# Kernel tuning notes

Hardware: AMD Instinct MI355X
Metric: run time of the kernel (lower is better)

The kernel has to match this reference:

```python
import jax, jax.numpy as jnp
import numpy as np


def _conv_same(x, w, b):
    # 3x3 same-padding conv, NCHW / OIHW (matches ConvNdWithSamePadding with
    # kernel=3, stride=1, dilation=1 -> symmetric pad of 1)
    y = jax.lax.conv_general_dilated(
        x, w, window_strides=(1, 1), padding='SAME',
        dimension_numbers=('NCHW', 'OIHW', 'NCHW'))
    return y + b[None, :, None, None]


def setup_inputs() -> dict:
    key = jax.random.key(0)
    ks = jax.random.split(key, 5)
    B, A, C, H, W = 8, 6, 256, 32, 32
    x = jax.random.normal(ks[0], (B, A, C, H, W), dtype=jnp.float32)
    w_ih = jax.random.normal(ks[1], (3 * C, 2 * C, 3, 3), dtype=jnp.float32) * 0.02
    w_hh = jax.random.normal(ks[2], (3 * C, C, 3, 3), dtype=jnp.float32) * 0.02
    b_ih = jax.random.normal(ks[3], (3 * C,), dtype=jnp.float32) * 0.02
    b_hh = jax.random.normal(ks[4], (3 * C,), dtype=jnp.float32) * 0.02
    return {'x': x, 'w_ih': w_ih, 'w_hh': w_hh, 'b_ih': b_ih, 'b_hh': b_hh,
            'num_iters': 3}


def reference(x, w_ih, w_hh, b_ih, b_hh, num_iters):
    # x: [B, A, C, H, W] per-agent BEV features.
    # Each GNN iteration: message = mean of other agents' features,
    # GRU input = concat(own, message) [2C ch], hidden = own feature [C ch],
    # new feature = ConvGRU cell output.
    B, A, C, H, W = x.shape
    for _ in range(num_iters):
        # mean over the other A-1 agents, computed via total sum (vectorized)
        msg = (jnp.sum(x, axis=1, keepdims=True) - x) / (A - 1)
        inp = jnp.concatenate([x, msg], axis=2).reshape(B * A, 2 * C, H, W)
        h = x.reshape(B * A, C, H, W)
        gi = _conv_same(inp, w_ih, b_ih)   # [B*A, 3C, H, W]
        gh = _conv_same(h, w_hh, b_hh)     # [B*A, 3C, H, W]
        i_r, i_i, i_n = jnp.split(gi, 3, axis=1)
        h_r, h_i, h_n = jnp.split(gh, 3, axis=1)
        resetgate = jax.nn.sigmoid(i_r + h_r)
        inputgate = jax.nn.sigmoid(i_i + h_i)
        newgate = jnp.tanh(i_n + resetgate * h_n)
        hy = newgate + inputgate * (h - newgate)
        x = hy.reshape(B, A, C, H, W)
    return x
```

## Files before the change

### kernel.cpp

```cpp
#include <hip/hip_runtime.h>
#include <stdint.h>

typedef unsigned short u16;
typedef __attribute__((ext_vector_type(8))) short short8;
typedef __attribute__((ext_vector_type(4))) float f32x4;

__device__ __forceinline__ u16 f2bf(float f) {
  uint32_t u = __builtin_bit_cast(uint32_t, f);
  u += 0x7fffu + ((u >> 16) & 1u);
  return (u16)(u >> 16);
}

__device__ __forceinline__ void gld16(const void* g, void* l) {
  __builtin_amdgcn_global_load_lds(
      (const __attribute__((address_space(1))) void*)g,
      (__attribute__((address_space(3))) void*)l, 16, 0, 0);
}

__device__ __forceinline__ void waitv(int n) {
  switch (n) {
    case 0: asm volatile("s_waitcnt vmcnt(0)" ::: "memory"); break;
    case 1: asm volatile("s_waitcnt vmcnt(1)" ::: "memory"); break;
    case 2: asm volatile("s_waitcnt vmcnt(2)" ::: "memory"); break;
    case 3: asm volatile("s_waitcnt vmcnt(3)" ::: "memory"); break;
    case 4: asm volatile("s_waitcnt vmcnt(4)" ::: "memory"); break;
    case 5: asm volatile("s_waitcnt vmcnt(5)" ::: "memory"); break;
    default: asm volatile("s_waitcnt vmcnt(6)" ::: "memory"); break;
  }
}

__global__ __launch_bounds__(256) void k_wprep(const float* __restrict__ w_ih,
                                               const float* __restrict__ w_hh,
                                               u16* __restrict__ wA,
                                               u16* __restrict__ wS) {
  const int NA = 8*9*8*192*32;
  const int NS = 8*9*8*96*32;
  for (int idx = blockIdx.x*blockDim.x + threadIdx.x; idx < NA + NS;
       idx += gridDim.x*blockDim.x) {
    if (idx < NA) {
      int kk = idx & 31; int t = idx >> 5;
      int nl = t % 192; t /= 192;
      int kb = t & 7; t >>= 3;
      int tap = t % 9; int cb = t / 9;
      int qq = nl / 96; int rr = nl % 96;
      int g = rr >> 4, cl = rr & 15;
      int c = cb*32 + qq*16 + cl, ci = kb*32 + kk;
      float v;
      if (g < 3) {
        int o = g*256 + c;
        v = w_ih[(o*512 + ci)*9 + tap] - 0.2f * w_ih[(o*512 + 256 + ci)*9 + tap];
      } else {
        int o = (g-3)*256 + c;
        v = w_hh[(o*256 + ci)*9 + tap];
      }
      wA[idx] = f2bf(v);
    } else {
      int j = idx - NA;
      int kk = j & 31; int t = j >> 5;
      int nl = t % 96; t /= 96;
      int kb = t & 7; t >>= 3;
      int tap = t % 9; int cb = t / 9;
      int o = cb*96 + nl, ci = kb*32 + kk;
      wS[j] = f2bf(0.2f * w_ih[(o*512 + 256 + ci)*9 + tap]);
    }
  }
}

__global__ __launch_bounds__(256) void k_xform(const float* __restrict__ src,
                                               u16* __restrict__ xbf,
                                               u16* __restrict__ sbf) {
  __shared__ float lds[32][33];
  const int t = threadIdx.x;
  const int tx = t & 31, ty = t >> 5;
  const int p0 = blockIdx.x*32, c0 = blockIdx.y*32, b = blockIdx.z;
  const int po = t >> 3, co = (t & 7)*4;
  float ss[4] = {0.f,0.f,0.f,0.f};
  for (int a = 0; a < 6; ++a) {
    const int im = b*6 + a;
    const float* sp = src + ((size_t)im*256 + c0)*1024 + p0;
    #pragma unroll
    for (int k = 0; k < 4; ++k) {
      float v = sp[(size_t)(ty + 8*k)*1024 + tx];
      ss[k] += v;
      lds[ty + 8*k][tx] = v;
    }
    __syncthreads();
    ushort4 pk = make_ushort4(f2bf(lds[co+0][po]), f2bf(lds[co+1][po]),
                              f2bf(lds[co+2][po]), f2bf(lds[co+3][po]));
    *(ushort4*)(xbf + ((size_t)im*1024 + p0+po)*256 + c0 + co) = pk;
    __syncthreads();
  }
  #pragma unroll
  for (int k = 0; k < 4; ++k) lds[ty + 8*k][tx] = ss[k];
  __syncthreads();
  ushort4 pk = make_ushort4(f2bf(lds[co+0][po]), f2bf(lds[co+1][po]),
                            f2bf(lds[co+2][po]), f2bf(lds[co+3][po]));
  *(ushort4*)(sbf + ((size_t)b*1024 + p0+po)*256 + c0 + co) = pk;
}

template<int GF, bool GATES>
__global__ __launch_bounds__(512, 2)
void k_conv(const u16* __restrict__ xin, const u16* __restrict__ wpre,
            float* __restrict__ gsbuf,
            const float* __restrict__ b_ih, const float* __restrict__ b_hh,
            const float* __restrict__ h_in, float* __restrict__ h_out) {
  constexpr int NT   = 512;
  constexpr int SLAB = 10*32*32;
  constexpr int BN   = 2*GF*16*32;
  constexpr int TOTA = 10*128;
  constexpr int TOTB = BN/8;
  __shared__ __align__(16) u16 slab[2][SLAB];
  __shared__ __align__(16) u16 bbuf[3][BN];

  const int tid = threadIdx.x;
  const int l  = tid & 63;
  const int w  = tid >> 6;
  const int lx = l & 15;
  const int lk = l >> 4;
  const int rg = w >> 1;
  const int q  = w & 1;

  int bid = blockIdx.x;
  const int cb = bid & 7; bid >>= 3;
  const int mt = bid & 3;
  const int img = bid >> 2;
  const int h0 = mt * 8;

  const u16* srcimg = xin + (size_t)img * (1024*256);

  const int trf = __builtin_amdgcn_readfirstlane(tid);
  const int myB = TOTB/NT + ((trf < (TOTB % NT)) ? 1 : 0);
  const int myA = TOTA/NT + ((trf < (TOTA % NT)) ? 1 : 0);

  auto stageA = [&](int kb, int sbuf) {
    #pragma unroll
    for (int ii = 0; ii < (TOTA + NT - 1)/NT; ++ii) {
      int i = ii*NT + tid;
      if (i < TOTA) {
        int p = i >> 2, ck = i & 3;
        int pr = p >> 5, pc = p & 31;
        int gr = h0 - 1 + pr;
        gr = gr < 0 ? 0 : (gr > 31 ? 31 : gr);
        int sck = ck ^ ((p >> 1) & 3);
        gld16(srcimg + (gr*32 + pc)*256 + kb*32 + sck*8, &slab[sbuf][i*8]);
      }
    }
  };
  auto stageB = [&](int kb, int tap, int bb) {
    const u16* wb = wpre + (size_t)((cb*9 + tap)*8 + kb) * BN;
    #pragma unroll
    for (int ii = 0; ii < (TOTB + NT - 1)/NT; ++ii) {
      int i = ii*NT + tid;
      if (i < TOTB) {
        int nl = i >> 2, ck = i & 3;
        int sck = ck ^ ((nl >> 1) & 3);
        gld16(wb + nl*32 + sck*8, &bbuf[bb][i*8]);
      }
    }
  };

  f32x4 acc[4][GF];
  #pragma unroll
  for (int mi = 0; mi < 4; ++mi)
    #pragma unroll
    for (int g = 0; g < GF; ++g) acc[mi][g] = (f32x4){0.f,0.f,0.f,0.f};

  stageA(0, 0);
  stageB(0, 0, 0);
  stageB(0, 1, 1);

  for (int kb = 0; kb < 8; ++kb) {
    const int sb = kb & 1;
    #pragma unroll
    for (int tap = 0; tap < 9; ++tap) {
      const int tau = kb*9 + tap;
      if (tau == 71) waitv(0);
      else if (tap == 7 && kb < 7) waitv(myA + myB);
      else waitv(myB);
      __builtin_amdgcn_s_barrier();
      __builtin_amdgcn_sched_barrier(0);

      if (tap == 6 && kb < 7) stageA(kb+1, sb^1);
      if (tau <= 69) stageB((tau+2)/9, (tau+2)%9, (tau+2)%3);

      const int dy = tap/3, dx = tap%3;
      short8 a[4];
      #pragma unroll
      for (int mi = 0; mi < 4; ++mi) {
        const int grow = h0 + rg*2 + (mi>>1) + dy - 1;
        const int cc = (mi&1)*16 + lx + dx - 1;
        const bool ok = (grow >= 0) && (grow < 32) && (cc >= 0) && (cc < 32);
        const int ccc = cc < 0 ? 0 : (cc > 31 ? 31 : cc);
        const int sr = rg*2 + (mi>>1) + dy;
        short8 av = *(const short8*)&slab[sb][(sr*32 + ccc)*32 + (lk ^ ((ccc >> 1) & 3))*8];
        if (!ok) av = (short8){0,0,0,0,0,0,0,0};
        a[mi] = av;
      }
      const u16* bp = &bbuf[tau % 3][(q*(GF*16) + lx)*32 + (lk ^ ((lx >> 1) & 3))*8];
      __builtin_amdgcn_s_setprio(1);
      #pragma unroll
      for (int g = 0; g < GF; ++g) {
        short8 bv = *(const short8*)(bp + g*(16*32));
        #pragma unroll
        for (int mi = 0; mi < 4; ++mi)
          acc[mi][g] = __builtin_amdgcn_mfma_f32_16x16x32_bf16(a[mi], bv, acc[mi][g], 0, 0, 0);
      }
      __builtin_amdgcn_s_setprio(0);
    }
  }

  if constexpr (GATES) {
    const int b = img / 6;
    const int c = cb*32 + q*16 + lx;
    const float bir = b_ih[c],  bii = b_ih[256+c], bin_ = b_ih[512+c];
    const float bhr = b_hh[c],  bhi = b_hh[256+c], bhn  = b_hh[512+c];
    const float* gs0 = gsbuf + ((size_t)(b*3+0)*256 + c)*1024;
    const float* gs1 = gsbuf + ((size_t)(b*3+1)*256 + c)*1024;
    const float* gs2 = gsbuf + ((size_t)(b*3+2)*256 + c)*1024;
    const float* hp  = h_in  + ((size_t)img*256 + c)*1024;
    float*       op  = h_out + ((size_t)img*256 + c)*1024;
    #pragma unroll
    for (int mi = 0; mi < 4; ++mi) {
      const int R = h0 + rg*2 + (mi>>1);
      const int pix = R*32 + (mi&1)*16 + lk*4;
      float4 v0 = *(const float4*)(gs0 + pix);
      float4 v1 = *(const float4*)(gs1 + pix);
      float4 v2 = *(const float4*)(gs2 + pix);
      float4 hv = *(const float4*)(hp + pix);
      float4 o;
      #pragma unroll
      for (int r = 0; r < 4; ++r) {
        float ir  = acc[mi][0][r] + (&v0.x)[r] + bir;
        float ii  = acc[mi][1][r] + (&v1.x)[r] + bii;
        float inn = acc[mi][2][r] + (&v2.x)[r] + bin_;
        float hr  = acc[mi][3][r] + bhr;
        float hi2 = acc[mi][4][r] + bhi;
        float hn  = acc[mi][5][r] + bhn;
        float rgt = 1.f/(1.f + __expf(-(ir+hr)));
        float igt = 1.f/(1.f + __expf(-(ii+hi2)));
        float nx = inn + rgt*hn;
        nx = nx > 20.f ? 20.f : (nx < -20.f ? -20.f : nx);
        float e2 = __expf(-2.f*nx);
        float ng = (1.f - e2)/(1.f + e2);
        (&o.x)[r] = ng + igt*((&hv.x)[r] - ng);
      }
      *(float4*)(op + pix) = o;
    }
  } else {
    #pragma unroll
    for (int g = 0; g < GF; ++g) {
      const int n = cb*(2*GF*16) + q*(GF*16) + g*16 + lx;
      float* gp = gsbuf + ((size_t)img*768 + n)*1024;
      #pragma unroll
      for (int mi = 0; mi < 4; ++mi) {
        const int R = h0 + rg*2 + (mi>>1);
        const int pix = R*32 + (mi&1)*16 + lk*4;
        *(float4*)(gp + pix) = make_float4(acc[mi][g][0], acc[mi][g][1],
                                           acc[mi][g][2], acc[mi][g][3]);
      }
    }
  }
}

extern "C" void kernel_launch(void* const* d_in, const int* in_sizes, int n_in,
                              void* d_out, int out_size, void* d_ws, size_t ws_size,
                              hipStream_t stream) {
  const float* x    = (const float*)d_in[0];
  const float* w_ih = (const float*)d_in[1];
  const float* w_hh = (const float*)d_in[2];
  const float* b_ih = (const float*)d_in[3];
  const float* b_hh = (const float*)d_in[4];
  float* out = (float*)d_out;

  char* ws = (char*)d_ws;
  float* m0  = (float*)(ws);
  u16*  xbf  = (u16*)(ws + 50331648);
  u16*  sbf  = (u16*)(ws + 75497472);
  float* gsb = (float*)(ws + 79691776);
  u16*  wA   = (u16*)(ws + 104857600);
  u16*  wS   = (u16*)(ws + 111935488);

  k_wprep<<<2048, 256, 0, stream>>>(w_ih, w_hh, wA, wS);

  for (int it = 0; it < 3; ++it) {
    const float* src = (it == 0) ? x : (it == 1 ? out : m0);
    float* dst = (it == 1) ? m0 : out;
    k_xform<<<dim3(32, 8, 8), 256, 0, stream>>>(src, xbf, sbf);
    k_conv<3, false><<<256, 512, 0, stream>>>(sbf, wS, gsb,
                                              nullptr, nullptr, nullptr, nullptr);
    k_conv<6, true><<<1536, 512, 0, stream>>>(xbf, wA, gsb,
                                              b_ih, b_hh, src, dst);
  }
}
```

Before: 1.541 ms.

## Switch conv kernels to 32x32x16 MFMA with larger row tiles and lane-swizzled gates

Replaces the 16x16x32 bf16 MFMA implicit-GEMM conv with a 32x32x16 variant. Each wave now covers a full 32-pixel row and 96 output columns, and the weight layout is reordered so input-gate and hidden-gate columns interleave per 16-channel group. The gated kernel tiles 16 rows per block (768 blocks instead of 1536), halving redundant halo and weight staging. It uses ds_swizzle to exchange ih and hh partial sums between lane halves for the GRU epilogue, and out-of-bounds pixels read from a zeroed LDS pad. The costs are more register pressure from 16-wide accumulators and fewer blocks for latency hiding.

```diff
diff --git a/kernel.cpp b/kernel.cpp
--- a/kernel.cpp
+++ b/kernel.cpp
@@ -3,7 +3,7 @@
 
 typedef unsigned short u16;
 typedef __attribute__((ext_vector_type(8))) short short8;
-typedef __attribute__((ext_vector_type(4))) float f32x4;
+typedef __attribute__((ext_vector_type(16))) float f32x16;
 
 __device__ __forceinline__ u16 f2bf(float f) {
   uint32_t u = __builtin_bit_cast(uint32_t, f);
@@ -25,7 +25,8 @@
     case 3: asm volatile("s_waitcnt vmcnt(3)" ::: "memory"); break;
     case 4: asm volatile("s_waitcnt vmcnt(4)" ::: "memory"); break;
     case 5: asm volatile("s_waitcnt vmcnt(5)" ::: "memory"); break;
-    default: asm volatile("s_waitcnt vmcnt(6)" ::: "memory"); break;
+    case 6: asm volatile("s_waitcnt vmcnt(6)" ::: "memory"); break;
+    default: asm volatile("s_waitcnt vmcnt(7)" ::: "memory"); break;
   }
 }
 
@@ -42,17 +43,15 @@
       int nl = t % 192; t /= 192;
       int kb = t & 7; t >>= 3;
       int tap = t % 9; int cb = t / 9;
-      int qq = nl / 96; int rr = nl % 96;
-      int g = rr >> 4, cl = rr & 15;
-      int c = cb*32 + qq*16 + cl, ci = kb*32 + kk;
+      int nh = nl / 96; int r2 = nl % 96;
+      int p = r2 >> 5, gp = (r2 >> 4) & 1, cl = r2 & 15;
+      int c = cb*32 + nh*16 + cl, ci = kb*32 + kk;
+      int o = p*256 + c;
       float v;
-      if (g < 3) {
-        int o = g*256 + c;
+      if (gp == 0)
         v = w_ih[(o*512 + ci)*9 + tap] - 0.2f * w_ih[(o*512 + 256 + ci)*9 + tap];
-      } else {
-        int o = (g-3)*256 + c;
+      else
         v = w_hh[(o*256 + ci)*9 + tap];
-      }
       wA[idx] = f2bf(v);
     } else {
       int j = idx - NA;
@@ -60,7 +59,8 @@
       int nl = t % 96; t /= 96;
       int kb = t & 7; t >>= 3;
       int tap = t % 9; int cb = t / 9;
-      int o = cb*96 + nl, ci = kb*32 + kk;
+      int p = nl >> 5, cl = nl & 31;
+      int o = p*256 + cb*32 + cl, ci = kb*32 + kk;
       wS[j] = f2bf(0.2f * w_ih[(o*512 + 256 + ci)*9 + tap]);
     }
   }
@@ -98,165 +98,213 @@
   *(ushort4*)(sbf + ((size_t)b*1024 + p0+po)*256 + c0 + co) = pk;
 }
 
-template<int GF, bool GATES>
+template<int MT, int NH, bool GATES>
 __global__ __launch_bounds__(512, 2)
-void k_conv(const u16* __restrict__ xin, const u16* __restrict__ wpre,
-            float* __restrict__ gsbuf,
-            const float* __restrict__ b_ih, const float* __restrict__ b_hh,
-            const float* __restrict__ h_in, float* __restrict__ h_out) {
-  constexpr int NT   = 512;
-  constexpr int SLAB = 10*32*32;
-  constexpr int BN   = 2*GF*16*32;
-  constexpr int TOTA = 10*128;
-  constexpr int TOTB = BN/8;
-  __shared__ __align__(16) u16 slab[2][SLAB];
-  __shared__ __align__(16) u16 bbuf[3][BN];
+void k_conv32(const u16* __restrict__ xin, const u16* __restrict__ wpre,
+              float* __restrict__ gsbuf,
+              const float* __restrict__ b_ih, const float* __restrict__ b_hh,
+              const float* __restrict__ h_in, float* __restrict__ h_out) {
+  constexpr int RGC   = 8 / NH;
+  constexpr int ROWS  = MT * RGC;
+  constexpr int MTC   = 32 / ROWS;
+  constexpr int NBLK  = 96 * NH;
+  constexpr int SLABR = ROWS + 2;
+  constexpr int SLABSZ = SLABR * 1024;
+  constexpr int BBSZ   = NBLK * 32;
+  constexpr int ZOFF   = 2*SLABSZ + 3*BBSZ;
+  constexpr int TOTA   = SLABR * 128;
+  constexpr int TOTB   = NBLK * 4;
+  __shared__ __align__(16) u16 L[ZOFF + 64];
 
   const int tid = threadIdx.x;
-  const int l  = tid & 63;
-  const int w  = tid >> 6;
-  const int lx = l & 15;
-  const int lk = l >> 4;
-  const int rg = w >> 1;
-  const int q  = w & 1;
+  const int l   = tid & 63;
+  const int w   = tid >> 6;
+  const int rg  = w / NH;
+  const int nh  = w % NH;
+  const int colc = l & 31;
+  const int kch  = l >> 5;
 
   int bid = blockIdx.x;
-  const int cb = bid & 7; bid >>= 3;
-  const int mt = bid & 3;
-  const int img = bid >> 2;
-  const int h0 = mt * 8;
+  const int cb  = bid & 7;
+  const int rest = bid >> 3;
+  const int mt  = rest % MTC;
+  const int img = rest / MTC;
+  const int h0  = mt * ROWS;
 
   const u16* srcimg = xin + (size_t)img * (1024*256);
 
   const int trf = __builtin_amdgcn_readfirstlane(tid);
-  const int myB = TOTB/NT + ((trf < (TOTB % NT)) ? 1 : 0);
-  const int myA = TOTA/NT + ((trf < (TOTA % NT)) ? 1 : 0);
+  const int myA = TOTA/512 + ((trf < (TOTA % 512)) ? 1 : 0);
+  const int myB = TOTB/512 + ((trf < (TOTB % 512)) ? 1 : 0);
 
   auto stageA = [&](int kb, int sbuf) {
     #pragma unroll
-    for (int ii = 0; ii < (TOTA + NT - 1)/NT; ++ii) {
-      int i = ii*NT + tid;
+    for (int ii = 0; ii < (TOTA + 511)/512; ++ii) {
+      int i = ii*512 + tid;
       if (i < TOTA) {
         int p = i >> 2, ck = i & 3;
         int pr = p >> 5, pc = p & 31;
         int gr = h0 - 1 + pr;
         gr = gr < 0 ? 0 : (gr > 31 ? 31 : gr);
-        int sck = ck ^ ((p >> 1) & 3);
-        gld16(srcimg + (gr*32 + pc)*256 + kb*32 + sck*8, &slab[sbuf][i*8]);
+        int sck = ck ^ ((pc >> 1) & 3);
+        gld16(srcimg + (gr*32 + pc)*256 + kb*32 + sck*8, &L[sbuf*SLABSZ + i*8]);
       }
     }
   };
   auto stageB = [&](int kb, int tap, int bb) {
-    const u16* wb = wpre + (size_t)((cb*9 + tap)*8 + kb) * BN;
-    #pragma unroll
-    for (int ii = 0; ii < (TOTB + NT - 1)/NT; ++ii) {
-      int i = ii*NT + tid;
+    const u16* wb = wpre + (size_t)((cb*9 + tap)*8 + kb) * BBSZ;
+    #pragma unroll
+    for (int ii = 0; ii < (TOTB + 511)/512; ++ii) {
+      int i = ii*512 + tid;
       if (i < TOTB) {
         int nl = i >> 2, ck = i & 3;
         int sck = ck ^ ((nl >> 1) & 3);
-        gld16(wb + nl*32 + sck*8, &bbuf[bb][i*8]);
+        gld16(wb + nl*32 + sck*8, &L[2*SLABSZ + bb*BBSZ + i*8]);
       }
     }
   };
 
-  f32x4 acc[4][GF];
+  f32x16 acc[MT][3];
   #pragma unroll
-  for (int mi = 0; mi < 4; ++mi)
-    #pragma unroll
-    for (int g = 0; g < GF; ++g) acc[mi][g] = (f32x4){0.f,0.f,0.f,0.f};
-
+  for (int mi = 0; mi < MT; ++mi)
+    #pragma unroll
+    for (int t = 0; t < 3; ++t)
+      #pragma unroll
+      for (int e = 0; e < 16; ++e) acc[mi][t][e] = 0.f;
+
+  if (tid < 64) L[ZOFF + tid] = 0;
   stageA(0, 0);
   stageB(0, 0, 0);
   stageB(0, 1, 1);
+  asm volatile("s_waitcnt lgkmcnt(0)" ::: "memory");
+
+  const int bkey = (colc >> 1) & 3;
+  const int bln  = (nh*96 + colc) * 32;
 
   for (int kb = 0; kb < 8; ++kb) {
     const int sb = kb & 1;
     #pragma unroll
     for (int tap = 0; tap < 9; ++tap) {
-      const int tau = kb*9 + tap;
-      if (tau == 71) waitv(0);
+      if (kb == 7 && tap == 8) waitv(0);
       else if (tap == 7 && kb < 7) waitv(myA + myB);
       else waitv(myB);
       __builtin_amdgcn_s_barrier();
       __builtin_amdgcn_sched_barrier(0);
 
       if (tap == 6 && kb < 7) stageA(kb+1, sb^1);
-      if (tau <= 69) stageB((tau+2)/9, (tau+2)%9, (tau+2)%3);
+      if (kb < 7 || tap < 7) {
+        const int kb2 = (tap < 7) ? kb : kb+1;
+        const int tp2 = (tap < 7) ? tap+2 : tap-7;
+        stageB(kb2, tp2, (tap+2) % 3);
+      }
 
       const int dy = tap/3, dx = tap%3;
-      short8 a[4];
-      #pragma unroll
-      for (int mi = 0; mi < 4; ++mi) {
-        const int grow = h0 + rg*2 + (mi>>1) + dy - 1;
-        const int cc = (mi&1)*16 + lx + dx - 1;
-        const bool ok = (grow >= 0) && (grow < 32) && (cc >= 0) && (cc < 32);
-        const int ccc = cc < 0 ? 0 : (cc > 31 ? 31 : cc);
-        const int sr = rg*2 + (mi>>1) + dy;
-        short8 av = *(const short8*)&slab[sb][(sr*32 + ccc)*32 + (lk ^ ((ccc >> 1) & 3))*8];
-        if (!ok) av = (short8){0,0,0,0,0,0,0,0};
-        a[mi] = av;
-      }
-      const u16* bp = &bbuf[tau % 3][(q*(GF*16) + lx)*32 + (lk ^ ((lx >> 1) & 3))*8];
+      const int cc = colc + dx - 1;
+      const bool colok = (unsigned)cc < 32u;
+      const int akey = (cc >> 1) & 3;
+      const int cc32 = cc * 32;
+      const int sbb = sb * SLABSZ;
+      const u16* bp0 = &L[2*SLABSZ + (tap%3)*BBSZ + bln];
+
       __builtin_amdgcn_s_setprio(1);
       #pragma unroll
-      for (int g = 0; g < GF; ++g) {
-        short8 bv = *(const short8*)(bp + g*(16*32));
+      for (int ks = 0; ks < 2; ++ks) {
+        const int c2 = ks*2 + kch;
+        const int ach = (c2 ^ akey) * 8;
+        const int bch = (c2 ^ bkey) * 8;
+        short8 b0 = *(const short8*)(bp0 + bch);
+        short8 b1 = *(const short8*)(bp0 + bch + 1024);
+        short8 b2 = *(const short8*)(bp0 + bch + 2048);
         #pragma unroll
-        for (int mi = 0; mi < 4; ++mi)
-          acc[mi][g] = __builtin_amdgcn_mfma_f32_16x16x32_bf16(a[mi], bv, acc[mi][g], 0, 0, 0);
+        for (int mi = 0; mi < MT; ++mi) {
+          const int rr = rg*MT + mi + dy;
+          const int grow = h0 + rr - 1;
+          const bool ok = ((unsigned)grow < 32u) && colok;
+          int aidx = sbb + rr*1024 + cc32 + ach;
+          aidx = ok ? aidx : ZOFF;
+          short8 av = *(const short8*)&L[aidx];
+          acc[mi][0] = __builtin_amdgcn_mfma_f32_32x32x16_bf16(av, b0, acc[mi][0], 0, 0, 0);
+          acc[mi][1] = __builtin_amdgcn_mfma_f32_32x32x16_bf16(av, b1, acc[mi][1], 0, 0, 0);
+          acc[mi][2] = __builtin_amdgcn_mfma_f32_32x32x16_bf16(av, b2, acc[mi][2], 0, 0, 0);
+        }
       }
       __builtin_amdgcn_s_setprio(0);
     }
   }
 
   if constexpr (GATES) {
-    const int b = img / 6;
-    const int c = cb*32 + q*16 + lx;
-    const float bir = b_ih[c],  bii = b_ih[256+c], bin_ = b_ih[512+c];
-    const float bhr = b_hh[c],  bhi = b_hh[256+c], bhn  = b_hh[512+c];
-    const float* gs0 = gsbuf + ((size_t)(b*3+0)*256 + c)*1024;
-    const float* gs1 = gsbuf + ((size_t)(b*3+1)*256 + c)*1024;
-    const float* gs2 = gsbuf + ((size_t)(b*3+2)*256 + c)*1024;
-    const float* hp  = h_in  + ((size_t)img*256 + c)*1024;
-    float*       op  = h_out + ((size_t)img*256 + c)*1024;
-    #pragma unroll
-    for (int mi = 0; mi < 4; ++mi) {
-      const int R = h0 + rg*2 + (mi>>1);
-      const int pix = R*32 + (mi&1)*16 + lk*4;
-      float4 v0 = *(const float4*)(gs0 + pix);
-      float4 v1 = *(const float4*)(gs1 + pix);
-      float4 v2 = *(const float4*)(gs2 + pix);
-      float4 hv = *(const float4*)(hp + pix);
-      float4 o;
+    const int gp2 = (l >> 4) & 1;
+    const int cl  = l & 15;
+    const int hx  = l >> 5;
+    const int cch = cb*32 + nh*16 + cl;
+    const int bat = img / 6;
+    float bI[3], bH[3];
+    #pragma unroll
+    for (int p = 0; p < 3; ++p) { bI[p] = b_ih[p*256 + cch]; bH[p] = b_hh[p*256 + cch]; }
+    const float* gs0 = gsbuf + ((size_t)(bat*3+0)*256 + cch)*1024;
+    const float* gs1 = gsbuf + ((size_t)(bat*3+1)*256 + cch)*1024;
+    const float* gs2 = gsbuf + ((size_t)(bat*3+2)*256 + cch)*1024;
+    const float* hp  = h_in  + ((size_t)img*256 + cch)*1024;
+    float*       op  = h_out + ((size_t)img*256 + cch)*1024;
+    #pragma unroll
+    for (int mi = 0; mi < MT; ++mi) {
+      const int R = h0 + rg*MT + mi;
+      const int px0 = R*32 + gp2*16 + hx*4;
+      float4 Ga0 = *(const float4*)(gs0 + px0), Gb0 = *(const float4*)(gs0 + px0 + 8);
+      float4 Ga1 = *(const float4*)(gs1 + px0), Gb1 = *(const float4*)(gs1 + px0 + 8);
+      float4 Ga2 = *(const float4*)(gs2 + px0), Gb2 = *(const float4*)(gs2 + px0 + 8);
+      float4 Ha  = *(const float4*)(hp + px0),  Hb  = *(const float4*)(hp + px0 + 8);
+      float4 Oa, Ob;
       #pragma unroll
-      for (int r = 0; r < 4; ++r) {
-        float ir  = acc[mi][0][r] + (&v0.x)[r] + bir;
-        float ii  = acc[mi][1][r] + (&v1.x)[r] + bii;
-        float inn = acc[mi][2][r] + (&v2.x)[r] + bin_;
-        float hr  = acc[mi][3][r] + bhr;
-        float hi2 = acc[mi][4][r] + bhi;
-        float hn  = acc[mi][5][r] + bhn;
+      for (int j = 0; j < 8; ++j) {
+        const int jj = j & 3;
+        float iv[3], hv[3];
+        #pragma unroll
+        for (int p = 0; p < 3; ++p) {
+          float own = gp2 ? acc[mi][p][8+j] : acc[mi][p][j];
+          float snd = gp2 ? acc[mi][p][j]   : acc[mi][p][8+j];
+          int gi = __builtin_amdgcn_ds_swizzle(__builtin_bit_cast(int, snd), 0x401F);
+          float got = __builtin_bit_cast(float, gi);
+          iv[p] = gp2 ? got : own;
+          hv[p] = gp2 ? own : got;
+        }
+        float g0 = (j < 4) ? (&Ga0.x)[jj] : (&Gb0.x)[jj];
+        float g1 = (j < 4) ? (&Ga1.x)[jj] : (&Gb1.x)[jj];
+        float g2 = (j < 4) ? (&Ga2.x)[jj] : (&Gb2.x)[jj];
+        float hold = (j < 4) ? (&Ha.x)[jj] : (&Hb.x)[jj];
+        float ir  = iv[0] + g0 + bI[0];
+        float ii  = iv[1] + g1 + bI[1];
+        float inn = iv[2] + g2 + bI[2];
+        float hr  = hv[0] + bH[0];
+        float hi2 = hv[1] + bH[1];
+        float hn  = hv[2] + bH[2];
         float rgt = 1.f/(1.f + __expf(-(ir+hr)));
         float igt = 1.f/(1.f + __expf(-(ii+hi2)));
         float nx = inn + rgt*hn;
         nx = nx > 20.f ? 20.f : (nx < -20.f ? -20.f : nx);
         float e2 = __expf(-2.f*nx);
         float ng = (1.f - e2)/(1.f + e2);
-        (&o.x)[r] = ng + igt*((&hv.x)[r] - ng);
-      }
-      *(float4*)(op + pix) = o;
+        float hy = ng + igt*(hold - ng);
+        if (j < 4) (&Oa.x)[jj] = hy; else (&Ob.x)[jj] = hy;
+      }
+      *(float4*)(op + px0) = Oa;
+      *(float4*)(op + px0 + 8) = Ob;
     }
   } else {
-    #pragma unroll
-    for (int g = 0; g < GF; ++g) {
-      const int n = cb*(2*GF*16) + q*(GF*16) + g*16 + lx;
-      float* gp = gsbuf + ((size_t)img*768 + n)*1024;
+    const int ch = cb*32 + colc;
+    const int hx = l >> 5;
+    #pragma unroll
+    for (int mi = 0; mi < MT; ++mi) {
+      const int R = h0 + rg*MT + mi;
       #pragma unroll
-      for (int mi = 0; mi < 4; ++mi) {
-        const int R = h0 + rg*2 + (mi>>1);
-        const int pix = R*32 + (mi&1)*16 + lk*4;
-        *(float4*)(gp + pix) = make_float4(acc[mi][g][0], acc[mi][g][1],
-                                           acc[mi][g][2], acc[mi][g][3]);
+      for (int p = 0; p < 3; ++p) {
+        float* gd = gsbuf + ((size_t)(img*3+p)*256 + ch)*1024;
+        #pragma unroll
+        for (int grp = 0; grp < 4; ++grp) {
+          float4 v = make_float4(acc[mi][p][grp*4+0], acc[mi][p][grp*4+1],
+                                 acc[mi][p][grp*4+2], acc[mi][p][grp*4+3]);
+          *(float4*)(gd + R*32 + grp*8 + hx*4) = v;
+        }
       }
     }
   }
@@ -286,9 +334,9 @@
     const float* src = (it == 0) ? x : (it == 1 ? out : m0);
     float* dst = (it == 1) ? m0 : out;
     k_xform<<<dim3(32, 8, 8), 256, 0, stream>>>(src, xbf, sbf);
-    k_conv<3, false><<<256, 512, 0, stream>>>(sbf, wS, gsb,
-                                              nullptr, nullptr, nullptr, nullptr);
-    k_conv<6, true><<<1536, 512, 0, stream>>>(xbf, wA, gsb,
-                                              b_ih, b_hh, src, dst);
-  }
-}
+    k_conv32<1, 1, false><<<256, 512, 0, stream>>>(sbf, wS, gsb,
+                                                   nullptr, nullptr, nullptr, nullptr);
+    k_conv32<4, 2, true><<<768, 512, 0, stream>>>(xbf, wA, gsb,
+                                                  b_ih, b_hh, src, dst);
+  }
+}
```

Result: slower. 2.197 ms (+42.6%).

## Prefetch next tap's LDS fragments into registers and deepen weight ring to four

Applied to the files above, without the earlier changes.

The conv main loop now reads the A and B fragments for the next tap from LDS into registers while the MFMAs for the current tap run, so LDS read latency overlaps with matrix math. The weight staging ring grows from three to four buffers and prefetches three taps ahead, and the sched_barrier is removed so the compiler can interleave the work. This costs more LDS and VGPRs, which may hurt occupancy at launch bounds of 2 blocks per CU.

```diff
diff --git a/kernel.cpp b/kernel.cpp
--- a/kernel.cpp
+++ b/kernel.cpp
@@ -110,7 +110,7 @@
   constexpr int TOTA = 10*128;
   constexpr int TOTB = BN/8;
   __shared__ __align__(16) u16 slab[2][SLAB];
-  __shared__ __align__(16) u16 bbuf[3][BN];
+  __shared__ __align__(16) u16 bbuf[4][BN];
 
   const int tid = threadIdx.x;
   const int l  = tid & 63;
@@ -159,53 +159,78 @@
     }
   };
 
+  auto loadA = [&](short8 (&a)[4], int DY, int DX, int ssel) {
+    #pragma unroll
+    for (int mi = 0; mi < 4; ++mi) {
+      const int grow = h0 + rg*2 + (mi>>1) + DY - 1;
+      const int cc = (mi&1)*16 + lx + DX - 1;
+      const bool ok = (grow >= 0) && (grow < 32) && (cc >= 0) && (cc < 32);
+      const int ccc = cc < 0 ? 0 : (cc > 31 ? 31 : cc);
+      const int sr = rg*2 + (mi>>1) + DY;
+      short8 av = *(const short8*)&slab[ssel][(sr*32 + ccc)*32 + (lk ^ ((ccc >> 1) & 3))*8];
+      if (!ok) av = (short8){0,0,0,0,0,0,0,0};
+      a[mi] = av;
+    }
+  };
+  auto loadB = [&](short8 (&b)[GF], int bb) {
+    const u16* bp = &bbuf[bb][(q*(GF*16) + lx)*32 + (lk ^ ((lx >> 1) & 3))*8];
+    #pragma unroll
+    for (int g = 0; g < GF; ++g) b[g] = *(const short8*)(bp + g*512);
+  };
+
   f32x4 acc[4][GF];
   #pragma unroll
   for (int mi = 0; mi < 4; ++mi)
     #pragma unroll
     for (int g = 0; g < GF; ++g) acc[mi][g] = (f32x4){0.f,0.f,0.f,0.f};
 
+  short8 a_cur[4], b_cur[GF], a_nxt[4], b_nxt[GF];
+
   stageA(0, 0);
   stageB(0, 0, 0);
   stageB(0, 1, 1);
+  stageB(0, 2, 2);
+  waitv(myB);
+  __builtin_amdgcn_s_barrier();
+  loadA(a_cur, 0, 0, 0);
+  loadB(b_cur, 0);
 
   for (int kb = 0; kb < 8; ++kb) {
     const int sb = kb & 1;
     #pragma unroll
     for (int tap = 0; tap < 9; ++tap) {
-      const int tau = kb*9 + tap;
-      if (tau == 71) waitv(0);
-      else if (tap == 7 && kb < 7) waitv(myA + myB);
-      else waitv(myB);
+      if (tap == 7)      { if (kb < 7) waitv(myA + myB); else waitv(0); }
+      else if (tap == 8) { if (kb < 7) waitv(myB);       else waitv(0); }
+      else               waitv(myB);
       __builtin_amdgcn_s_barrier();
-      __builtin_amdgcn_sched_barrier(0);
 
       if (tap == 6 && kb < 7) stageA(kb+1, sb^1);
-      if (tau <= 69) stageB((tau+2)/9, (tau+2)%9, (tau+2)%3);
-
-      const int dy = tap/3, dx = tap%3;
-      short8 a[4];
-      #pragma unroll
-      for (int mi = 0; mi < 4; ++mi) {
-        const int grow = h0 + rg*2 + (mi>>1) + dy - 1;
-        const int cc = (mi&1)*16 + lx + dx - 1;
-        const bool ok = (grow >= 0) && (grow < 32) && (cc >= 0) && (cc < 32);
-        const int ccc = cc < 0 ? 0 : (cc > 31 ? 31 : cc);
-        const int sr = rg*2 + (mi>>1) + dy;
-        short8 av = *(const short8*)&slab[sb][(sr*32 + ccc)*32 + (lk ^ ((ccc >> 1) & 3))*8];
-        if (!ok) av = (short8){0,0,0,0,0,0,0,0};
-        a[mi] = av;
-      }
-      const u16* bp = &bbuf[tau % 3][(q*(GF*16) + lx)*32 + (lk ^ ((lx >> 1) & 3))*8];
+      if (kb*9 + tap <= 68) {
+        const int kb2 = (tap < 6) ? kb : kb+1;
+        const int tp2 = (tap < 6) ? tap+3 : tap-6;
+        stageB(kb2, tp2, (kb*9 + tap + 3) & 3);
+      }
+
+      if (tap < 8) {
+        loadA(a_nxt, (tap+1)/3, (tap+1)%3, sb);
+        loadB(b_nxt, (kb*9 + tap + 1) & 3);
+      } else if (kb < 7) {
+        loadA(a_nxt, 0, 0, sb^1);
+        loadB(b_nxt, (kb*9 + tap + 1) & 3);
+      }
+
       __builtin_amdgcn_s_setprio(1);
       #pragma unroll
-      for (int g = 0; g < GF; ++g) {
-        short8 bv = *(const short8*)(bp + g*(16*32));
+      for (int g = 0; g < GF; ++g)
         #pragma unroll
         for (int mi = 0; mi < 4; ++mi)
-          acc[mi][g] = __builtin_amdgcn_mfma_f32_16x16x32_bf16(a[mi], bv, acc[mi][g], 0, 0, 0);
-      }
+          acc[mi][g] = __builtin_amdgcn_mfma_f32_16x16x32_bf16(a_cur[mi], b_cur[g], acc[mi][g], 0, 0, 0);
       __builtin_amdgcn_s_setprio(0);
+
+      #pragma unroll
+      for (int mi = 0; mi < 4; ++mi) a_cur[mi] = a_nxt[mi];
+      #pragma unroll
+      for (int g = 0; g < GF; ++g)  b_cur[g] = b_nxt[g];
     }
   }
 
```

New measurement: 1.859 ms. 20.7% more time.

## Retile conv blocks to one row per wave and raise occupancy bound

Applied to the files above, without the earlier changes.

The conv kernel is reparameterised by NQ, the number of channel quarters. Each wave now computes one output row (2 M-tiles) against 6 N-groups, instead of 2 rows against GF groups. The gated conv now uses 4-row tiles, which doubles its grid. Launch bounds rise to 4 blocks per CU so that more waves can be resident and hide latency. In exchange, each B fragment loaded from LDS is reused by only 2 MFMAs, halo rows are a larger share of each smaller tile, and the tighter register budget may cause spills.

```diff
diff --git a/kernel.cpp b/kernel.cpp
--- a/kernel.cpp
+++ b/kernel.cpp
@@ -98,17 +98,21 @@
   *(ushort4*)(sbf + ((size_t)b*1024 + p0+po)*256 + c0 + co) = pk;
 }
 
-template<int GF, bool GATES>
-__global__ __launch_bounds__(512, 2)
+template<int NQ, bool GATES>
+__global__ __launch_bounds__(512, 4)
 void k_conv(const u16* __restrict__ xin, const u16* __restrict__ wpre,
             float* __restrict__ gsbuf,
             const float* __restrict__ b_ih, const float* __restrict__ b_hh,
             const float* __restrict__ h_in, float* __restrict__ h_out) {
-  constexpr int NT   = 512;
-  constexpr int SLAB = 10*32*32;
-  constexpr int BN   = 2*GF*16*32;
-  constexpr int TOTA = 10*128;
-  constexpr int TOTB = BN/8;
+  constexpr int NT    = 512;
+  constexpr int RB    = 8 / NQ;
+  constexpr int MTC   = 32 / RB;
+  constexpr int SLABR = RB + 2;
+  constexpr int SLAB  = SLABR*32*32;
+  constexpr int NBLK  = NQ*96;
+  constexpr int BN    = NBLK*32;
+  constexpr int TOTA  = SLABR*128;
+  constexpr int TOTB  = BN/8;
   __shared__ __align__(16) u16 slab[2][SLAB];
   __shared__ __align__(16) u16 bbuf[3][BN];
 
@@ -117,14 +121,15 @@
   const int w  = tid >> 6;
   const int lx = l & 15;
   const int lk = l >> 4;
-  const int rg = w >> 1;
-  const int q  = w & 1;
+  const int rg = w / NQ;
+  const int q  = w % NQ;
 
   int bid = blockIdx.x;
-  const int cb = bid & 7; bid >>= 3;
-  const int mt = bid & 3;
-  const int img = bid >> 2;
-  const int h0 = mt * 8;
+  const int cb = bid & 7;
+  const int rest = bid >> 3;
+  const int mt = rest % MTC;
+  const int img = rest / MTC;
+  const int h0 = mt * RB;
 
   const u16* srcimg = xin + (size_t)img * (1024*256);
 
@@ -159,11 +164,11 @@
     }
   };
 
-  f32x4 acc[4][GF];
+  f32x4 acc[2][6];
   #pragma unroll
-  for (int mi = 0; mi < 4; ++mi)
-    #pragma unroll
-    for (int g = 0; g < GF; ++g) acc[mi][g] = (f32x4){0.f,0.f,0.f,0.f};
+  for (int mi = 0; mi < 2; ++mi)
+    #pragma unroll
+    for (int g = 0; g < 6; ++g) acc[mi][g] = (f32x4){0.f,0.f,0.f,0.f};
 
   stageA(0, 0);
   stageB(0, 0, 0);
@@ -184,26 +189,26 @@
       if (tau <= 69) stageB((tau+2)/9, (tau+2)%9, (tau+2)%3);
 
       const int dy = tap/3, dx = tap%3;
-      short8 a[4];
-      #pragma unroll
-      for (int mi = 0; mi < 4; ++mi) {
-        const int grow = h0 + rg*2 + (mi>>1) + dy - 1;
-        const int cc = (mi&1)*16 + lx + dx - 1;
-        const bool ok = (grow >= 0) && (grow < 32) && (cc >= 0) && (cc < 32);
+      const int grow = h0 + rg + dy - 1;
+      const bool rowok = (grow >= 0) && (grow < 32);
+      const int sr = rg + dy;
+      short8 a[2];
+      #pragma unroll
+      for (int mi = 0; mi < 2; ++mi) {
+        const int cc = mi*16 + lx + dx - 1;
+        const bool ok = rowok && (cc >= 0) && (cc < 32);
         const int ccc = cc < 0 ? 0 : (cc > 31 ? 31 : cc);
-        const int sr = rg*2 + (mi>>1) + dy;
         short8 av = *(const short8*)&slab[sb][(sr*32 + ccc)*32 + (lk ^ ((ccc >> 1) & 3))*8];
         if (!ok) av = (short8){0,0,0,0,0,0,0,0};
         a[mi] = av;
       }
-      const u16* bp = &bbuf[tau % 3][(q*(GF*16) + lx)*32 + (lk ^ ((lx >> 1) & 3))*8];
+      const u16* bp = &bbuf[tau % 3][(q*96 + lx)*32 + (lk ^ ((lx >> 1) & 3))*8];
       __builtin_amdgcn_s_setprio(1);
       #pragma unroll
-      for (int g = 0; g < GF; ++g) {
-        short8 bv = *(const short8*)(bp + g*(16*32));
-        #pragma unroll
-        for (int mi = 0; mi < 4; ++mi)
-          acc[mi][g] = __builtin_amdgcn_mfma_f32_16x16x32_bf16(a[mi], bv, acc[mi][g], 0, 0, 0);
+      for (int g = 0; g < 6; ++g) {
+        short8 bv = *(const short8*)(bp + g*512);
+        acc[0][g] = __builtin_amdgcn_mfma_f32_16x16x32_bf16(a[0], bv, acc[0][g], 0, 0, 0);
+        acc[1][g] = __builtin_amdgcn_mfma_f32_16x16x32_bf16(a[1], bv, acc[1][g], 0, 0, 0);
       }
       __builtin_amdgcn_s_setprio(0);
     }
@@ -219,10 +224,10 @@
     const float* gs2 = gsbuf + ((size_t)(b*3+2)*256 + c)*1024;
     const float* hp  = h_in  + ((size_t)img*256 + c)*1024;
     float*       op  = h_out + ((size_t)img*256 + c)*1024;
-    #pragma unroll
-    for (int mi = 0; mi < 4; ++mi) {
-      const int R = h0 + rg*2 + (mi>>1);
-      const int pix = R*32 + (mi&1)*16 + lk*4;
+    const int R = h0 + rg;
+    #pragma unroll
+    for (int mi = 0; mi < 2; ++mi) {
+      const int pix = R*32 + mi*16 + lk*4;
       float4 v0 = *(const float4*)(gs0 + pix);
       float4 v1 = *(const float4*)(gs1 + pix);
       float4 v2 = *(const float4*)(gs2 + pix);
@@ -247,14 +252,14 @@
       *(float4*)(op + pix) = o;
     }
   } else {
-    #pragma unroll
-    for (int g = 0; g < GF; ++g) {
-      const int n = cb*(2*GF*16) + q*(GF*16) + g*16 + lx;
+    const int R = h0 + rg;
+    #pragma unroll
+    for (int g = 0; g < 6; ++g) {
+      const int n = cb*NBLK + q*96 + g*16 + lx;
       float* gp = gsbuf + ((size_t)img*768 + n)*1024;
       #pragma unroll
-      for (int mi = 0; mi < 4; ++mi) {
-        const int R = h0 + rg*2 + (mi>>1);
-        const int pix = R*32 + (mi&1)*16 + lk*4;
+      for (int mi = 0; mi < 2; ++mi) {
+        const int pix = R*32 + mi*16 + lk*4;
         *(float4*)(gp + pix) = make_float4(acc[mi][g][0], acc[mi][g][1],
                                            acc[mi][g][2], acc[mi][g][3]);
       }
@@ -286,9 +291,9 @@
     const float* src = (it == 0) ? x : (it == 1 ? out : m0);
     float* dst = (it == 1) ? m0 : out;
     k_xform<<<dim3(32, 8, 8), 256, 0, stream>>>(src, xbf, sbf);
-    k_conv<3, false><<<256, 512, 0, stream>>>(sbf, wS, gsb,
+    k_conv<1, false><<<256, 512, 0, stream>>>(sbf, wS, gsb,
                                               nullptr, nullptr, nullptr, nullptr);
-    k_conv<6, true><<<1536, 512, 0, stream>>>(xbf, wA, gsb,
+    k_conv<2, true><<<3072, 512, 0, stream>>>(xbf, wA, gsb,
                                               b_ih, b_hh, src, dst);
   }
 }
```

Result: faster. 1.318 ms (-14.4%).
